# Kernel tuning notes

Hardware: AMD Instinct MI355X
Metric: run time of the kernel (lower is better)

Reference implementation:

```python
import jax, jax.numpy as jnp
import numpy as np

B, S, D = 4, 2048, 1024
H, HD = 16, 64  # n_heads, head_dim; D == H*HD


def setup_inputs() -> dict:
    key = jax.random.key(0)
    k1, k2, k3, k4, k5 = jax.random.split(key, 5)
    s = 0.02
    return {
        "x": jax.random.normal(k1, (B, S, D), dtype=jnp.float32),
        "w_qkv": jax.random.normal(k2, (D, 3 * D), dtype=jnp.float32) * s,
        "b_qkv": jax.random.normal(k3, (3 * D,), dtype=jnp.float32) * s,
        "w_out": jax.random.normal(k4, (D, D), dtype=jnp.float32) * s,
        "b_out": jax.random.normal(k5, (D,), dtype=jnp.float32) * s,
    }


def reference(x, w_qkv, b_qkv, w_out, b_out):
    b, s, d = x.shape
    qkv = x @ w_qkv + b_qkv                      # [B,S,3D]
    qkv = qkv.reshape(b, s, 3, H, HD)
    qkv = jnp.transpose(qkv, (2, 0, 3, 1, 4))    # [3,B,H,S,HD]
    q, k, v = qkv[0], qkv[1], qkv[2]
    scale = 1.0 / np.sqrt(HD).astype(np.float32)
    scores = jnp.einsum("bhqd,bhkd->bhqk", q, k) * scale  # [B,H,S,S]
    causal = jnp.tril(jnp.ones((s, s), dtype=bool))
    scores = jnp.where(causal[None, None], scores, -jnp.inf)
    weights = jax.nn.softmax(scores, axis=-1)
    attn = jnp.einsum("bhqk,bhkd->bhqd", weights, v)       # [B,H,S,HD]
    attn = jnp.transpose(attn, (0, 2, 1, 3)).reshape(b, s, d)
    return attn @ w_out + b_out
```

## Files before the change

kernel.cpp:

```cpp
#include <hip/hip_runtime.h>
#include <hip/hip_bf16.h>

#define B_DIM 4
#define S_DIM 2048
#define D_DIM 1024
#define H_DIM 16
#define HD_DIM 64

using bf16 = __hip_bfloat16;
using bf16x8 = __attribute__((ext_vector_type(8))) short;
using f32x4 = __attribute__((ext_vector_type(4))) float;

__device__ inline unsigned short f2bfu(float f) {
    bf16 h = __float2bfloat16(f);
    unsigned short s;
    __builtin_memcpy(&s, &h, 2);
    return s;
}
__device__ inline unsigned int pack2bf(float a, float b) {
    return (unsigned int)f2bfu(a) | ((unsigned int)f2bfu(b) << 16);
}
__device__ inline float exp2_raw(float x) {
    float r;
    asm("v_exp_f32 %0, %1" : "=v"(r) : "v"(x));
    return r;
}

typedef __attribute__((address_space(1))) const void cg_void;
typedef __attribute__((address_space(3))) void lds_void;
__device__ inline void gload_lds16(const void* g, void* l) {
    __builtin_amdgcn_global_load_lds((cg_void*)g, (lds_void*)l, 16, 0, 0);
}

__global__ __launch_bounds__(256) void conv_bf16_kernel(const float* __restrict__ in,
                                                        bf16* __restrict__ out, int n4) {
    int i = blockIdx.x * 256 + threadIdx.x;
    if (i >= n4) return;
    float4 v = reinterpret_cast<const float4*>(in)[i];
    ushort4 o;
    o.x = f2bfu(v.x); o.y = f2bfu(v.y); o.z = f2bfu(v.z); o.w = f2bfu(v.w);
    reinterpret_cast<ushort4*>(out)[i] = o;
}

__global__ __launch_bounds__(256) void transpose_bf16_kernel(const float* __restrict__ in,
                                                             bf16* __restrict__ out,
                                                             int R, int C) {
    __shared__ float tile[32][33];
    int c0 = blockIdx.x * 32, r0 = blockIdx.y * 32;
    int tx = threadIdx.x, ty = threadIdx.y;
#pragma unroll
    for (int i = 0; i < 32; i += 8)
        tile[ty + i][tx] = in[(size_t)(r0 + ty + i) * C + c0 + tx];
    __syncthreads();
#pragma unroll
    for (int i = 0; i < 32; i += 8)
        out[(size_t)(c0 + ty + i) * R + r0 + tx] = __float2bfloat16(tile[tx][ty + i]);
}

#define GEMM_PREAMBLE()                                                        \
    const int K = D_DIM;                                                       \
    __shared__ __align__(16) char smem[65536];                                 \
    int m0 = blockIdx.y * 128;                                                 \
    int n0 = blockIdx.x * 128;                                                 \
    int tid = threadIdx.x;                                                     \
    int lane = tid & 63;                                                       \
    int w = tid >> 6;                                                          \
    int wr = w >> 1, wc = w & 1;                                               \
    int lr = lane & 15, lk = lane >> 4;                                        \
    f32x4 acc[4][4] = {};                                                      \
    int sr8 = lane >> 3;                                     \
    int scol = (((lane & 7) * 16) ^ (sr8 << 4)) >> 1;    \
    int wub = w * 1024;                                                        \
    const int rsw = (lr & 7) << 4;                                             \
    const bf16* Arow = A + (size_t)(m0 + w * 8 + sr8) * K + scol;              \
    const bf16* Brow = BT + (size_t)(n0 + w * 8 + sr8) * K + scol;

#define GEMM_STAGE(buf, kk)                                                    \
    do {                                                                       \
        char* ab_ = smem + (buf) * 32768;                                      \
        gload_lds16(Arow + (kk), ab_ + wub);                                   \
        gload_lds16(Arow + 32 * 1024 + (kk), ab_ + 4096 + wub);                \
        gload_lds16(Arow + 64 * 1024 + (kk), ab_ + 8192 + wub);                \
        gload_lds16(Arow + 96 * 1024 + (kk), ab_ + 12288 + wub);               \
        gload_lds16(Brow + (kk), ab_ + 16384 + wub);                           \
        gload_lds16(Brow + 32 * 1024 + (kk), ab_ + 20480 + wub);               \
        gload_lds16(Brow + 64 * 1024 + (kk), ab_ + 24576 + wub);               \
        gload_lds16(Brow + 96 * 1024 + (kk), ab_ + 28672 + wub);               \
    } while (0)

#define GEMM_MAINLOOP()                                                        \
    const int NT = K / 64;                                             \
    GEMM_STAGE(0, 0);                                                          \
    for (int t = 0; t < NT; ++t) {                                             \
        asm volatile("s_waitcnt vmcnt(0)" ::: "memory");                       \
        __builtin_amdgcn_s_barrier();                                          \
        __builtin_amdgcn_sched_barrier(0);                                     \
        if (t + 1 < NT) GEMM_STAGE((t + 1) & 1, (t + 1) * 64);                 \
        char* as = smem + (t & 1) * 32768;                                     \
        char* bs = as + 16384;                                                 \
        bf16x8 af[4][2], bfr[4][2];                                            \
        _Pragma("unroll")                                                      \
        for (int m = 0; m < 4; ++m) {                                          \
            int rb = (wr * 64 + m * 16 + lr) * 128;                            \
            af[m][0] = *(const bf16x8*)(as + rb + ((lk * 16) ^ rsw));          \
            af[m][1] = *(const bf16x8*)(as + rb + ((64 + lk * 16) ^ rsw));     \
        }                                                                      \
        _Pragma("unroll")                                                      \
        for (int n = 0; n < 4; ++n) {                                          \
            int rb = (wc * 64 + n * 16 + lr) * 128;                            \
            bfr[n][0] = *(const bf16x8*)(bs + rb + ((lk * 16) ^ rsw));         \
            bfr[n][1] = *(const bf16x8*)(bs + rb + ((64 + lk * 16) ^ rsw));    \
        }                                                                      \
        __builtin_amdgcn_s_setprio(1);                                         \
        _Pragma("unroll")                                                      \
        for (int m = 0; m < 4; ++m)                                            \
            _Pragma("unroll")                                                  \
            for (int n = 0; n < 4; ++n) {                                      \
                acc[m][n] = __builtin_amdgcn_mfma_f32_16x16x32_bf16(           \
                    af[m][0], bfr[n][0], acc[m][n], 0, 0, 0);                  \
                acc[m][n] = __builtin_amdgcn_mfma_f32_16x16x32_bf16(           \
                    af[m][1], bfr[n][1], acc[m][n], 0, 0, 0);                  \
            }                                                                  \
        __builtin_amdgcn_s_setprio(0);                                         \
    }

__global__ __launch_bounds__(256, 2) void gemm_qkv_kernel(const bf16* __restrict__ A,
                                                          const bf16* __restrict__ BT,
                                                          const float* __restrict__ bias,
                                                          bf16* __restrict__ Qo,
                                                          bf16* __restrict__ Ko,
                                                          bf16* __restrict__ Vt) {
    GEMM_PREAMBLE();
    GEMM_MAINLOOP();
    const float QS = 0.18033688f;
    int third = n0 >> 10;
#pragma unroll
    for (int m = 0; m < 4; ++m) {
        int row = m0 + wr * 64 + m * 16 + lk * 4;
        int b = row >> 11, s = row & 2047;
#pragma unroll
        for (int n = 0; n < 4; ++n) {
            int col = n0 + wc * 64 + n * 16 + lr;
            int rem = col & 1023;
            int h = rem >> 6, hd = rem & 63;
            float bv = bias[col];
            if (third == 0) {
#pragma unroll
                for (int i = 0; i < 4; ++i)
                    Qo[(((size_t)b * H_DIM + h) * S_DIM + s + i) * HD_DIM + hd] =
                        __float2bfloat16((acc[m][n][i] + bv) * QS);
            } else if (third == 1) {
#pragma unroll
                for (int i = 0; i < 4; ++i)
                    Ko[(((size_t)b * H_DIM + h) * S_DIM + s + i) * HD_DIM + hd] =
                        __float2bfloat16(acc[m][n][i] + bv);
            } else {
                uint2 d;
                d.x = pack2bf(acc[m][n][0] + bv, acc[m][n][1] + bv);
                d.y = pack2bf(acc[m][n][2] + bv, acc[m][n][3] + bv);
                *(uint2*)&Vt[(((size_t)b * H_DIM + h) * HD_DIM + hd) * S_DIM + s] = d;
            }
        }
    }
}

__global__ __launch_bounds__(256, 4) void attn_kernel(const bf16* __restrict__ Q,
                                                      const bf16* __restrict__ K,
                                                      const bf16* __restrict__ Vt,
                                                      bf16* __restrict__ Aout) {
    __shared__ __align__(16) char smem[40960];
    int bid = blockIdx.x;
    int bh = bid & 63;
    const int st_tbl[16] = {15, 14, 13, 12, 8, 9, 10, 11, 4, 5, 6, 7, 3, 2, 1, 0};
    int st = st_tbl[bid >> 6];
    int b = bh >> 4, h = bh & 15;
    int w = threadIdx.x >> 6;
    int lane = threadIdx.x & 63;
    int lr = lane & 15, lk = lane >> 4;

    const short* Qs = (const short*)(Q + (size_t)bh * S_DIM * HD_DIM);
    const short* Ks = (const short*)(K + (size_t)bh * S_DIM * HD_DIM);
    const short* Vs = (const short*)(Vt + (size_t)bh * HD_DIM * S_DIM);
    char* pb = smem + 32768 + w * 2048;
    const int sw = (lr & 7) << 4;

    int srow = w * 8 + (lane >> 3);
    int sblk = ((lane & 7) ^ (lane >> 3)) * 8;
    int wub = w * 1024;

    int q0w = st * 128 + w * 32;
    int nt = 2 * st + 2;
    int twl = 2 * st + ((w >> 1) & 1);

    bf16x8 qf[2][2];
#pragma unroll
    for (int qg = 0; qg < 2; ++qg)
#pragma unroll
        for (int c = 0; c < 2; ++c)
            qf[qg][c] = *(const bf16x8*)&Qs[(size_t)(q0w + qg * 16 + lr) * 64 + c * 32 + lk * 8];

    bf16x8 onesv;
#pragma unroll
    for (int z = 0; z < 8; ++z) onesv[z] = (short)0x3F80;

    f32x4 o[4][2] = {};
    f32x4 ol[2] = {};

    gload_lds16(Ks + (size_t)srow * 64 + sblk, smem + wub);
    gload_lds16(Ks + (size_t)(32 + srow) * 64 + sblk, smem + 4096 + wub);
    gload_lds16(Vs + (size_t)srow * S_DIM + sblk, smem + 16384 + wub);
    gload_lds16(Vs + (size_t)(32 + srow) * S_DIM + sblk, smem + 20480 + wub);

    for (int t = 0; t < nt; ++t) {
        int cur = t & 1;
        int kv0 = t * 64;
        __syncthreads();
        if (t + 1 < nt) {
            int kn = kv0 + 64;
            char* kd = smem + (cur ^ 1) * 8192;
            char* vd = smem + 16384 + (cur ^ 1) * 8192;
            gload_lds16(Ks + (size_t)(kn + srow) * 64 + sblk, kd + wub);
            gload_lds16(Ks + (size_t)(kn + 32 + srow) * 64 + sblk, kd + 4096 + wub);
            gload_lds16(Vs + (size_t)srow * S_DIM + kn + sblk, vd + wub);
            gload_lds16(Vs + (size_t)(32 + srow) * S_DIM + kn + sblk, vd + 4096 + wub);
        }
        if (t > twl) continue;
        char* kt = smem + cur * 8192;
        char* vt = smem + 16384 + cur * 8192;
        bool diag = (t == twl);
        int mhi = diag ? ((w & 1) ? 4 : 2) : 4;

        f32x4 s[4][2] = {};
        __builtin_amdgcn_s_setprio(1);
#pragma unroll
        for (int m = 0; m < 4; ++m) {
            if (m >= mhi) continue;
            int rb = (m * 16 + lr) * 128;
            bf16x8 ka = *(const bf16x8*)(kt + rb + ((lk * 16) ^ sw));
            bf16x8 kb2 = *(const bf16x8*)(kt + rb + ((64 + lk * 16) ^ sw));
            s[m][0] = __builtin_amdgcn_mfma_f32_16x16x32_bf16(ka, qf[0][0], s[m][0], 0, 0, 0);
            s[m][0] = __builtin_amdgcn_mfma_f32_16x16x32_bf16(kb2, qf[0][1], s[m][0], 0, 0, 0);
            s[m][1] = __builtin_amdgcn_mfma_f32_16x16x32_bf16(ka, qf[1][0], s[m][1], 0, 0, 0);
            s[m][1] = __builtin_amdgcn_mfma_f32_16x16x32_bf16(kb2, qf[1][1], s[m][1], 0, 0, 0);
        }
        __builtin_amdgcn_s_setprio(0);

        if (kv0 + 63 > q0w) {
#pragma unroll
            for (int m = 0; m < 4; ++m)
#pragma unroll
                for (int qg = 0; qg < 2; ++qg) {
                    int qq = q0w + qg * 16 + lr;
#pragma unroll
                    for (int i = 0; i < 4; ++i)
                        if (kv0 + m * 16 + lk * 4 + i > qq) s[m][qg][i] = -1e30f;
                }
        }

#pragma unroll
        for (int m = 0; m < 4; ++m)
#pragma unroll
            for (int qg = 0; qg < 2; ++qg)
#pragma unroll
                for (int i = 0; i < 4; ++i) s[m][qg][i] = exp2_raw(s[m][qg][i]);

        bf16x8 pf[2][2];
#pragma unroll
        for (int qg = 0; qg < 2; ++qg) {
#pragma unroll
            for (int m = 0; m < 4; ++m) {
                uint2 d;
                d.x = pack2bf(s[m][qg][0], s[m][qg][1]);
                d.y = pack2bf(s[m][qg][2], s[m][qg][3]);
                *(uint2*)(pb + lr * 128 + ((m * 32 + lk * 8) ^ sw)) = d;
            }
            pf[qg][0] = *(const bf16x8*)(pb + lr * 128 + ((lk * 16) ^ sw));
            pf[qg][1] = *(const bf16x8*)(pb + lr * 128 + ((64 + lk * 16) ^ sw));
        }

        __builtin_amdgcn_s_setprio(1);
#pragma unroll
        for (int m = 0; m < 4; ++m) {
            int rb = (m * 16 + lr) * 128;
            bf16x8 va = *(const bf16x8*)(vt + rb + ((lk * 16) ^ sw));
            bf16x8 vb2 = *(const bf16x8*)(vt + rb + ((64 + lk * 16) ^ sw));
            o[m][0] = __builtin_amdgcn_mfma_f32_16x16x32_bf16(va, pf[0][0], o[m][0], 0, 0, 0);
            o[m][0] = __builtin_amdgcn_mfma_f32_16x16x32_bf16(vb2, pf[0][1], o[m][0], 0, 0, 0);
            o[m][1] = __builtin_amdgcn_mfma_f32_16x16x32_bf16(va, pf[1][0], o[m][1], 0, 0, 0);
            o[m][1] = __builtin_amdgcn_mfma_f32_16x16x32_bf16(vb2, pf[1][1], o[m][1], 0, 0, 0);
        }
        ol[0] = __builtin_amdgcn_mfma_f32_16x16x32_bf16(onesv, pf[0][0], ol[0], 0, 0, 0);
        ol[0] = __builtin_amdgcn_mfma_f32_16x16x32_bf16(onesv, pf[0][1], ol[0], 0, 0, 0);
        ol[1] = __builtin_amdgcn_mfma_f32_16x16x32_bf16(onesv, pf[1][0], ol[1], 0, 0, 0);
        ol[1] = __builtin_amdgcn_mfma_f32_16x16x32_bf16(onesv, pf[1][1], ol[1], 0, 0, 0);
        __builtin_amdgcn_s_setprio(0);
    }

    short* op = (short*)Aout;
#pragma unroll
    for (int qg = 0; qg < 2; ++qg) {
        float inv = 1.0f / ol[qg][0];
        size_t orow = ((size_t)b * S_DIM + q0w + qg * 16 + lr) * D_DIM + h * 64;
#pragma unroll
        for (int m = 0; m < 4; ++m) {
            uint2 d;
            d.x = pack2bf(o[m][qg][0] * inv, o[m][qg][1] * inv);
            d.y = pack2bf(o[m][qg][2] * inv, o[m][qg][3] * inv);
            *(uint2*)(op + orow + m * 16 + lk * 4) = d;
        }
    }
}

__global__ __launch_bounds__(256, 2) void gemm_out_kernel(const bf16* __restrict__ A,
                                                          const bf16* __restrict__ BT,
                                                          const float* __restrict__ bias,
                                                          float* __restrict__ Out) {
    GEMM_PREAMBLE();
    GEMM_MAINLOOP();
#pragma unroll
    for (int m = 0; m < 4; ++m) {
        int row = m0 + wr * 64 + m * 16 + lk * 4;
#pragma unroll
        for (int n = 0; n < 4; ++n) {
            int col = n0 + wc * 64 + n * 16 + lr;
            float bv = bias[col];
#pragma unroll
            for (int i = 0; i < 4; ++i)
                Out[(size_t)(row + i) * D_DIM + col] = acc[m][n][i] + bv;
        }
    }
}

extern "C" void kernel_launch(void* const* d_in, const int* in_sizes, int n_in,
                              void* d_out, int out_size, void* d_ws, size_t ws_size,
                              hipStream_t stream) {
    const float* x = (const float*)d_in[0];
    const float* w_qkv = (const float*)d_in[1];
    const float* b_qkv = (const float*)d_in[2];
    const float* w_out = (const float*)d_in[3];
    const float* b_out = (const float*)d_in[4];
    float* out = (float*)d_out;

    char* ws = (char*)d_ws;
    const size_t SZ_X = (size_t)B_DIM * S_DIM * D_DIM * 2;
    const size_t SZ_WQKV = (size_t)D_DIM * 3 * D_DIM * 2;
    const size_t SZ_WOUT = (size_t)D_DIM * D_DIM * 2;
    bf16* xb = (bf16*)(ws);
    bf16* wqkvT = (bf16*)(ws + SZ_X);
    bf16* woutT = (bf16*)(ws + SZ_X + SZ_WQKV);
    bf16* Qb = (bf16*)(ws + SZ_X + SZ_WQKV + SZ_WOUT);
    bf16* Kb = (bf16*)(ws + SZ_X + SZ_WQKV + SZ_WOUT + SZ_X);
    bf16* Vtb = (bf16*)(ws + SZ_X + SZ_WQKV + SZ_WOUT + 2 * SZ_X);

    {
        int n4 = (B_DIM * S_DIM * D_DIM) / 4;
        conv_bf16_kernel<<<n4 / 256, 256, 0, stream>>>(x, xb, n4);
    }
    transpose_bf16_kernel<<<dim3(3 * D_DIM / 32, D_DIM / 32), dim3(32, 8), 0, stream>>>(
        w_qkv, wqkvT, D_DIM, 3 * D_DIM);
    transpose_bf16_kernel<<<dim3(D_DIM / 32, D_DIM / 32), dim3(32, 8), 0, stream>>>(
        w_out, woutT, D_DIM, D_DIM);
    gemm_qkv_kernel<<<dim3(3 * D_DIM / 128, B_DIM * S_DIM / 128), 256, 0, stream>>>(
        xb, wqkvT, b_qkv, Qb, Kb, Vtb);
    attn_kernel<<<dim3(B_DIM * H_DIM * 16), 256, 0, stream>>>(Qb, Kb, Vtb, xb);
    gemm_out_kernel<<<dim3(D_DIM / 128, B_DIM * S_DIM / 128), 256, 0, stream>>>(
        xb, woutT, b_out, out);
}
```

Before: 143.8 us.

## Split GEMM staging into A/B halves and remap blocks for XCD locality

The GEMM main loop now stages B and A tiles separately and waits on each with partial vmcnt counts. The second K-half MFMAs of one step are deferred and overlapped with the next step's loads and LDS reads, so global loads and compute interleave inside a tile. Launches become 1D, and block IDs are remapped so that each XCD (assumed 8, via bid & 7) handles a contiguous group of M rows, aiming to improve L2 reuse. The price is more barriers per iteration and extra live registers for the carried fragments, which may pressure the 2-blocks-per-CU occupancy.

```diff
diff --git a/kernel.cpp b/kernel.cpp
--- a/kernel.cpp
+++ b/kernel.cpp
@@ -60,8 +60,11 @@
 #define GEMM_PREAMBLE()                                                        \
     const int K = D_DIM;                                                       \
     __shared__ __align__(16) char smem[65536];                                 \
-    int m0 = blockIdx.y * 128;                                                 \
-    int n0 = blockIdx.x * 128;                                                 \
+    int bid3 = blockIdx.x;                                                     \
+    int xcd = bid3 & 7;                                                        \
+    int inner = bid3 >> 3;                                                     \
+    int m0 = ((xcd << 3) | (inner & 7)) * 128;        \
+    int n0 = (inner >> 3) * 128;                              \
     int tid = threadIdx.x;                                                     \
     int lane = tid & 63;                                                       \
     int w = tid >> 6;                                                          \
@@ -75,54 +78,85 @@
     const bf16* Arow = A + (size_t)(m0 + w * 8 + sr8) * K + scol;              \
     const bf16* Brow = BT + (size_t)(n0 + w * 8 + sr8) * K + scol;
 
-#define GEMM_STAGE(buf, kk)                                                    \
+#define GEMM_STAGE_A(buf, kk)                                                  \
     do {                                                                       \
-        char* ab_ = smem + (buf) * 32768;                                      \
-        gload_lds16(Arow + (kk), ab_ + wub);                                   \
-        gload_lds16(Arow + 32 * 1024 + (kk), ab_ + 4096 + wub);                \
-        gload_lds16(Arow + 64 * 1024 + (kk), ab_ + 8192 + wub);                \
-        gload_lds16(Arow + 96 * 1024 + (kk), ab_ + 12288 + wub);               \
-        gload_lds16(Brow + (kk), ab_ + 16384 + wub);                           \
-        gload_lds16(Brow + 32 * 1024 + (kk), ab_ + 20480 + wub);               \
-        gload_lds16(Brow + 64 * 1024 + (kk), ab_ + 24576 + wub);               \
-        gload_lds16(Brow + 96 * 1024 + (kk), ab_ + 28672 + wub);               \
+        char* aa_ = smem + (buf) * 32768;                                      \
+        gload_lds16(Arow + (kk), aa_ + wub);                                   \
+        gload_lds16(Arow + 32 * 1024 + (kk), aa_ + 4096 + wub);                \
+        gload_lds16(Arow + 64 * 1024 + (kk), aa_ + 8192 + wub);                \
+        gload_lds16(Arow + 96 * 1024 + (kk), aa_ + 12288 + wub);               \
+    } while (0)
+
+#define GEMM_STAGE_B(buf, kk)                                                  \
+    do {                                                                       \
+        char* bb_ = smem + (buf) * 32768 + 16384;                              \
+        gload_lds16(Brow + (kk), bb_ + wub);                                   \
+        gload_lds16(Brow + 32 * 1024 + (kk), bb_ + 4096 + wub);                \
+        gload_lds16(Brow + 64 * 1024 + (kk), bb_ + 8192 + wub);                \
+        gload_lds16(Brow + 96 * 1024 + (kk), bb_ + 12288 + wub);               \
     } while (0)
 
 #define GEMM_MAINLOOP()                                                        \
     const int NT = K / 64;                                             \
-    GEMM_STAGE(0, 0);                                                          \
+    GEMM_STAGE_B(0, 0);                                                        \
+    GEMM_STAGE_A(0, 0);                                                        \
+    bf16x8 af0[4], af1[4], bf0[4], bf1[4], pa1[4], pb1[4];                     \
     for (int t = 0; t < NT; ++t) {                                             \
-        asm volatile("s_waitcnt vmcnt(0)" ::: "memory");                       \
+        char* as = smem + (t & 1) * 32768;                                     \
+        char* bs = as + 16384;                                                 \
+              \
+        asm volatile("s_waitcnt vmcnt(4)" ::: "memory");                       \
         __builtin_amdgcn_s_barrier();                                          \
         __builtin_amdgcn_sched_barrier(0);                                     \
-        if (t + 1 < NT) GEMM_STAGE((t + 1) & 1, (t + 1) * 64);                 \
-        char* as = smem + (t & 1) * 32768;                                     \
-        char* bs = as + 16384;                                                 \
-        bf16x8 af[4][2], bfr[4][2];                                            \
+        _Pragma("unroll")                                                      \
+        for (int n = 0; n < 4; ++n) {                                          \
+            int rb = (wc * 64 + n * 16 + lr) * 128;                            \
+            bf0[n] = *(const bf16x8*)(bs + rb + ((lk * 16) ^ rsw));            \
+            bf1[n] = *(const bf16x8*)(bs + rb + ((64 + lk * 16) ^ rsw));       \
+        }                                                                      \
+        if (t + 1 < NT) GEMM_STAGE_B((t + 1) & 1, (t + 1) * 64);               \
+        if (t) {                                                               \
+            __builtin_amdgcn_s_setprio(1);                                     \
+            _Pragma("unroll")                                                  \
+            for (int m = 0; m < 4; ++m)                                        \
+                _Pragma("unroll")                                              \
+                for (int n = 0; n < 4; ++n)                                    \
+                    acc[m][n] = __builtin_amdgcn_mfma_f32_16x16x32_bf16(       \
+                        pa1[m], pb1[n], acc[m][n], 0, 0, 0);                   \
+            __builtin_amdgcn_s_setprio(0);                                     \
+        }                                                                      \
+                \
+        if (t + 1 < NT) asm volatile("s_waitcnt vmcnt(4)" ::: "memory");       \
+        else            asm volatile("s_waitcnt vmcnt(0)" ::: "memory");       \
+        __builtin_amdgcn_s_barrier();                                          \
+        __builtin_amdgcn_sched_barrier(0);                                     \
         _Pragma("unroll")                                                      \
         for (int m = 0; m < 4; ++m) {                                          \
             int rb = (wr * 64 + m * 16 + lr) * 128;                            \
-            af[m][0] = *(const bf16x8*)(as + rb + ((lk * 16) ^ rsw));          \
-            af[m][1] = *(const bf16x8*)(as + rb + ((64 + lk * 16) ^ rsw));     \
+            af0[m] = *(const bf16x8*)(as + rb + ((lk * 16) ^ rsw));            \
+            af1[m] = *(const bf16x8*)(as + rb + ((64 + lk * 16) ^ rsw));       \
         }                                                                      \
-        _Pragma("unroll")                                                      \
-        for (int n = 0; n < 4; ++n) {                                          \
-            int rb = (wc * 64 + n * 16 + lr) * 128;                            \
-            bfr[n][0] = *(const bf16x8*)(bs + rb + ((lk * 16) ^ rsw));         \
-            bfr[n][1] = *(const bf16x8*)(bs + rb + ((64 + lk * 16) ^ rsw));    \
-        }                                                                      \
+        if (t + 1 < NT) GEMM_STAGE_A((t + 1) & 1, (t + 1) * 64);               \
         __builtin_amdgcn_s_setprio(1);                                         \
         _Pragma("unroll")                                                      \
         for (int m = 0; m < 4; ++m)                                            \
             _Pragma("unroll")                                                  \
-            for (int n = 0; n < 4; ++n) {                                      \
+            for (int n = 0; n < 4; ++n)                                        \
                 acc[m][n] = __builtin_amdgcn_mfma_f32_16x16x32_bf16(           \
-                    af[m][0], bfr[n][0], acc[m][n], 0, 0, 0);                  \
-                acc[m][n] = __builtin_amdgcn_mfma_f32_16x16x32_bf16(           \
-                    af[m][1], bfr[n][1], acc[m][n], 0, 0, 0);                  \
-            }                                                                  \
+                    af0[m], bf0[n], acc[m][n], 0, 0, 0);                       \
         __builtin_amdgcn_s_setprio(0);                                         \
-    }
+        _Pragma("unroll")                                                      \
+        for (int m = 0; m < 4; ++m) pa1[m] = af1[m];                           \
+        _Pragma("unroll")                                                      \
+        for (int n = 0; n < 4; ++n) pb1[n] = bf1[n];                           \
+    }                                                                          \
+                                              \
+    _Pragma("unroll")                                                          \
+    for (int m = 0; m < 4; ++m)                                                \
+        _Pragma("unroll")                                                      \
+        for (int n = 0; n < 4; ++n)                                            \
+            acc[m][n] = __builtin_amdgcn_mfma_f32_16x16x32_bf16(               \
+                pa1[m], pb1[n], acc[m][n], 0, 0, 0);
 
 __global__ __launch_bounds__(256, 2) void gemm_qkv_kernel(const bf16* __restrict__ A,
                                                           const bf16* __restrict__ BT,
@@ -360,9 +394,7 @@
         w_qkv, wqkvT, D_DIM, 3 * D_DIM);
     transpose_bf16_kernel<<<dim3(D_DIM / 32, D_DIM / 32), dim3(32, 8), 0, stream>>>(
         w_out, woutT, D_DIM, D_DIM);
-    gemm_qkv_kernel<<<dim3(3 * D_DIM / 128, B_DIM * S_DIM / 128), 256, 0, stream>>>(
-        xb, wqkvT, b_qkv, Qb, Kb, Vtb);
+    gemm_qkv_kernel<<<1536, 256, 0, stream>>>(xb, wqkvT, b_qkv, Qb, Kb, Vtb);
     attn_kernel<<<dim3(B_DIM * H_DIM * 16), 256, 0, stream>>>(Qb, Kb, Vtb, xb);
-    gemm_out_kernel<<<dim3(D_DIM / 128, B_DIM * S_DIM / 128), 256, 0, stream>>>(
-        xb, woutT, b_out, out);
-}
+    gemm_out_kernel<<<512, 256, 0, stream>>>(xb, woutT, b_out, out);
+}
```

After: 136.4 us. -5.2%, faster.
